# Kernel tuning notes

Measured on AMD Instinct MI355X. Metric: run time of the kernel, lower is better.

Reference implementation:

```python
import jax, jax.numpy as jnp
import numpy as np

B, N, FIN, D, L, DF = 16, 768, 56, 140, 4, 128


def setup_inputs() -> dict:
    key = jax.random.key(0)
    ks = jax.random.split(key, 24)
    c_hs = jax.random.normal(ks[0], (B, N, FIN), jnp.float32)
    # receptor prefix length r, total atoms n (r < n <= N)
    r = jax.random.randint(ks[1], (B,), N // 4, N // 2)
    num_atoms = jax.random.randint(ks[2], (B,), (3 * N) // 4, N + 1).astype(jnp.int32)
    idx = jnp.arange(N)
    c_valid = (idx[None, :] < r[:, None]).astype(jnp.int32)
    # intra-molecule adjacency: sparse symmetric 0/1 with self loops
    a1 = (jax.random.uniform(ks[3], (B, N, N)) < 0.05).astype(jnp.float32)
    c_adjs1 = jnp.clip(jnp.maximum(a1, a1.transpose(0, 2, 1)) + jnp.eye(N, dtype=jnp.float32)[None], 0.0, 1.0)
    # cross distances in Angstroms
    d2 = jax.random.uniform(ks[4], (B, N, N), jnp.float32, 0.0, 20.0)
    c_adjs2 = 0.5 * (d2 + d2.transpose(0, 2, 1))
    s = 0.1
    params = dict(
        W_emb=s * jax.random.normal(ks[5], (FIN, D), jnp.float32),
        gat_W=s * jax.random.normal(ks[6], (L, D, D), jnp.float32),
        gat_Wb=jnp.zeros((L, D), jnp.float32),
        gat_A=s * jax.random.normal(ks[7], (L, D, D), jnp.float32),
        gat_gw=s * jax.random.normal(ks[8], (L, 2 * D, 1), jnp.float32),
        gat_gb=jnp.zeros((L, 1), jnp.float32),
        fc_w0=s * jax.random.normal(ks[9], (D, DF), jnp.float32),
        fc_b0=jnp.zeros((DF,), jnp.float32),
        fc_w1=s * jax.random.normal(ks[10], (DF, DF), jnp.float32),
        fc_b1=jnp.zeros((DF,), jnp.float32),
        fc_w2=s * jax.random.normal(ks[11], (DF, DF), jnp.float32),
        fc_b2=jnp.zeros((DF,), jnp.float32),
        fc_w3=s * jax.random.normal(ks[12], (DF, 1), jnp.float32),
        fc_b3=jnp.zeros((1,), jnp.float32),
        mu=jnp.array([4.0], jnp.float32),
        dev=jnp.array([1.0], jnp.float32),
    )
    return dict(c_hs=c_hs, c_adjs1=c_adjs1, c_adjs2=c_adjs2, c_valid=c_valid, num_atoms=num_atoms, **params)


def _formulate_adj2(adj2, c_valid, num_atoms, mu, dev):
    # vectorized version of the per-batch Python loop in Formulate_Adj2
    r = jnp.sum(c_valid > 0, axis=1)          # [B] receptor prefix length
    n = num_atoms                              # [B] total atoms
    i = jnp.arange(N)
    row_rec = i[None, :, None] < r[:, None, None]              # row < r
    col_lig = (i[None, None, :] >= r[:, None, None]) & (i[None, None, :] < n[:, None, None])
    maskA = row_rec & col_lig                  # [B,N,N] receptor-row x ligand-col block
    gauss = jnp.exp(-jnp.square(adj2 - mu) / dev)
    upd = jnp.where(adj2 <= 10.0, gauss, jnp.zeros_like(adj2))
    out = jnp.where(maskA, upd, adj2)
    out = jnp.where(maskA.transpose(0, 2, 1), out.transpose(0, 2, 1), out)  # symmetrize block
    return out


def _gat_gate(x, adj, W, Wb, A, gw, gb):
    h = x @ W + Wb                                             # [B,N,D]
    e = jnp.einsum('bjl,bkl->bjk', h @ A, h)                   # [B,N,N]
    e = e + e.transpose(0, 2, 1)
    att = jnp.where(adj > 0, e, jnp.float32(-9e15))
    att = jax.nn.softmax(att, axis=1)                          # NOTE: dim=1, as in torch code
    att = att * adj
    h_prime = jax.nn.relu(jnp.einsum('bij,bjk->bik', att, h))  # [B,N,D]
    coeff = jax.nn.sigmoid(jnp.concatenate([x, h_prime], -1) @ gw + gb)  # [B,N,1]
    return coeff * x + (1.0 - coeff) * h_prime


def reference(c_hs, c_adjs1, c_adjs2, c_valid, num_atoms, W_emb, gat_W, gat_Wb, gat_A, gat_gw, gat_gb,
              fc_w0, fc_b0, fc_w1, fc_b1, fc_w2, fc_b2, fc_w3, fc_b3, mu, dev):
    x = c_hs @ W_emb                                           # embede (no bias)
    adj2 = _formulate_adj2(c_adjs2, c_valid, num_atoms, mu, dev)
    for k in range(gat_W.shape[0]):                            # embede_graph (eval: dropout is identity)
        h1 = _gat_gate(x, c_adjs1, gat_W[k], gat_Wb[k], gat_A[k], gat_gw[k], gat_gb[k])
        h2 = _gat_gate(x, adj2, gat_W[k], gat_Wb[k], gat_A[k], gat_gw[k], gat_gb[k])
        x = h2 - h1
    # Get_Prediction: ragged sum pool over first num_atoms rows
    mask = (jnp.arange(N)[None, :] < num_atoms[:, None]).astype(x.dtype)
    pred = jnp.sum(x * mask[:, :, None], axis=1)               # [B,D]
    h = jax.nn.relu(pred @ fc_w0 + fc_b0)
    h = jax.nn.relu(h @ fc_w1 + fc_b1)
    h = jax.nn.relu(h @ fc_w2 + fc_b2)
    out = jax.nn.sigmoid(h @ fc_w3 + fc_b3)
    return out.reshape(-1)                                     # [B]
```

## Files before the change

kernel.cpp:

```cpp
#include <hip/hip_runtime.h>

constexpr int B   = 16;
constexpr int N   = 768;
constexpr int FIN = 56;
constexpr int D   = 140;
constexpr int L   = 4;
constexpr int DF  = 128;
constexpr int NN  = N * N;
constexpr int BND = B * N * D;
constexpr int BNN = B * NN;

constexpr int PROWS  = 16;
constexpr int NCHUNK = N / PROWS;

constexpr int NTILE = N / 64;
constexpr int NTRI  = NTILE * (NTILE + 1) / 2;

constexpr int JSPLIT = 8;

struct PartPtrs { float* p[JSPLIT]; };

template<int K>
__global__ __launch_bounds__(256) void k_linrb(const float* __restrict__ in,
                                               const float* __restrict__ W,
                                               const float* __restrict__ bias,
                                               float* __restrict__ out) {
    constexpr int NDG = D / 4;
    int idx = blockIdx.x * 256 + threadIdx.x;
    if (idx >= (B * N / 4) * NDG) return;
    int dt = idx % NDG;
    int rt = idx / NDG;
    int r0 = rt * 4, d = dt * 4;

    float acc[4][4];
    float b0 = 0.f, b1 = 0.f, b2 = 0.f, b3 = 0.f;
    if (bias) { b0 = bias[d]; b1 = bias[d + 1]; b2 = bias[d + 2]; b3 = bias[d + 3]; }
#pragma unroll
    for (int s = 0; s < 4; ++s) {
        acc[s][0] = b0; acc[s][1] = b1; acc[s][2] = b2; acc[s][3] = b3;
    }

#pragma unroll 2
    for (int k = 0; k < K; k += 4) {
        float4 wv[4];
#pragma unroll
        for (int kk = 0; kk < 4; ++kk)
            wv[kk] = *reinterpret_cast<const float4*>(&W[(size_t)(k + kk) * D + d]);
#pragma unroll
        for (int s = 0; s < 4; ++s) {
            float4 xv = *reinterpret_cast<const float4*>(&in[(size_t)(r0 + s) * K + k]);
            float xa[4] = {xv.x, xv.y, xv.z, xv.w};
#pragma unroll
            for (int kk = 0; kk < 4; ++kk) {
                acc[s][0] += xa[kk] * wv[kk].x;
                acc[s][1] += xa[kk] * wv[kk].y;
                acc[s][2] += xa[kk] * wv[kk].z;
                acc[s][3] += xa[kk] * wv[kk].w;
            }
        }
    }

#pragma unroll
    for (int s = 0; s < 4; ++s) {
        float4 v = {acc[s][0], acc[s][1], acc[s][2], acc[s][3]};
        *reinterpret_cast<float4*>(&out[(size_t)(r0 + s) * D + d]) = v;
    }
}

__global__ __launch_bounds__(256) void k_adj2(const float* __restrict__ a2,
                                              const int* __restrict__ valid,
                                              const int* __restrict__ natoms,
                                              const float* __restrict__ mu,
                                              const float* __restrict__ dev,
                                              float* __restrict__ out) {
    int idx = blockIdx.x * 256 + threadIdx.x;
    if (idx >= BNN) return;
    int b   = idx / NN;
    int rem = idx - b * NN;
    int i   = rem / N;
    int j   = rem - i * N;
    float a = a2[idx];
    int vi = valid[b * N + i];
    int vj = valid[b * N + j];
    int n  = natoms[b];
    bool mask = (vi && !vj && (j < n)) || (vj && !vi && (i < n));
    float dmu = a - mu[0];
    float g = (a <= 10.f) ? expf(-dmu * dmu / dev[0]) : 0.f;
    out[idx] = mask ? g : a;
}

__global__ __launch_bounds__(256) void k_e(const float* __restrict__ h,
                                           const float* __restrict__ hA,
                                           float* __restrict__ E) {
    int t = blockIdx.x;
    int b = blockIdx.y;
    int tj = 0, rem = t, rowlen = NTILE;
    while (rem >= rowlen) { rem -= rowlen; ++tj; --rowlen; }
    int tk = tj + rem;

    __shared__ float sJ[72][68];
    __shared__ float sK[72][68];
    int tid = threadIdx.x;
    int jg  = tid & 15;
    int kg  = tid >> 4;
    int j0 = tj * 64, k0 = tk * 64;
    const float* hb = h  + (size_t)b * N * D;
    const float* ab = hA + (size_t)b * N * D;

    float acc[4][4] = {};

    for (int r = 0; r < 4; ++r) {
        int ph = r >> 1;
        int c0 = (r & 1) ? 72 : 0;
        int kc = (r & 1) ? 68 : 72;
        int ncb = kc >> 2;
        const float* uS = ph ? hb : ab;
        const float* vS = ph ? ab : hb;
        if (r) __syncthreads();
        for (int idx = tid; idx < ncb * 16; idx += 256) {
            int cb = idx % ncb;
            int jb = (idx / ncb) * 4;
            int gc = c0 + cb * 4;
            float4 ru[4], rv[4];
#pragma unroll
            for (int s = 0; s < 4; ++s) {
                ru[s] = *reinterpret_cast<const float4*>(&uS[(size_t)(j0 + jb + s) * D + gc]);
                rv[s] = *reinterpret_cast<const float4*>(&vS[(size_t)(k0 + jb + s) * D + gc]);
            }
            float tu[4][4], tv[4][4];
#pragma unroll
            for (int s = 0; s < 4; ++s) {
                tu[s][0] = ru[s].x; tu[s][1] = ru[s].y; tu[s][2] = ru[s].z; tu[s][3] = ru[s].w;
                tv[s][0] = rv[s].x; tv[s][1] = rv[s].y; tv[s][2] = rv[s].z; tv[s][3] = rv[s].w;
            }
#pragma unroll
            for (int s = 0; s < 4; ++s) {
                float4 wu = {tu[0][s], tu[1][s], tu[2][s], tu[3][s]};
                float4 wv = {tv[0][s], tv[1][s], tv[2][s], tv[3][s]};
                *reinterpret_cast<float4*>(&sJ[cb * 4 + s][jb]) = wu;
                *reinterpret_cast<float4*>(&sK[cb * 4 + s][jb]) = wv;
            }
        }
        __syncthreads();
#pragma unroll 4
        for (int kk = 0; kk < kc; ++kk) {
            float4 ajv = *reinterpret_cast<const float4*>(&sJ[kk][jg * 4]);
            float4 akv = *reinterpret_cast<const float4*>(&sK[kk][kg * 4]);
            float aj[4] = {ajv.x, ajv.y, ajv.z, ajv.w};
            float ak[4] = {akv.x, akv.y, akv.z, akv.w};
#pragma unroll
            for (int i = 0; i < 4; ++i)
#pragma unroll
                for (int q = 0; q < 4; ++q) acc[i][q] += aj[i] * ak[q];
        }
    }

    float* Eb = E + (size_t)b * NN;
    int jb = j0 + jg * 4, kb = k0 + kg * 4;
#pragma unroll
    for (int i = 0; i < 4; ++i) {
        float4 v = {acc[i][0], acc[i][1], acc[i][2], acc[i][3]};
        *reinterpret_cast<float4*>(&Eb[(size_t)(jb + i) * N + kb]) = v;
    }
#pragma unroll
    for (int q = 0; q < 4; ++q) {
        float4 v = {acc[0][q], acc[1][q], acc[2][q], acc[3][q]};
        *reinterpret_cast<float4*>(&Eb[(size_t)(kb + q) * N + jb]) = v;
    }
}

__global__ __launch_bounds__(1024) void k_stats(const float* __restrict__ E,
                                                const float* __restrict__ a1,
                                                const float* __restrict__ a2,
                                                float* __restrict__ M1g, float* __restrict__ IS1g,
                                                float* __restrict__ M2g, float* __restrict__ IS2g) {
    int b    = blockIdx.y;
    int lane = threadIdx.x & 63;
    int js   = threadIdx.x >> 6;
    int k    = blockIdx.x * 64 + lane;
    const float* Eb = E  + (size_t)b * NN;
    const float* A1 = a1 + (size_t)b * NN;
    const float* A2 = a2 + (size_t)b * NN;

    float m1 = -3.0e38f, s1 = 0.f, m2 = -3.0e38f, s2 = 0.f;
    for (int j = js; j < N; j += 16) {
        float ev = Eb[(size_t)j * N + k];
        float v1 = A1[(size_t)j * N + k];
        float v2 = A2[(size_t)j * N + k];
        float x1 = (v1 > 0.f) ? ev : -9e15f;
        float x2 = (v2 > 0.f) ? ev : -9e15f;
        float n1 = fmaxf(m1, x1);
        s1 = s1 * __expf(m1 - n1) + __expf(x1 - n1);
        m1 = n1;
        float n2 = fmaxf(m2, x2);
        s2 = s2 * __expf(m2 - n2) + __expf(x2 - n2);
        m2 = n2;
    }
    __shared__ float sm1[16][64], ss1[16][64], sm2[16][64], ss2[16][64];
    sm1[js][lane] = m1; ss1[js][lane] = s1;
    sm2[js][lane] = m2; ss2[js][lane] = s2;
    __syncthreads();
    if (js == 0) {
        float M = sm1[0][lane], S = ss1[0][lane];
#pragma unroll
        for (int q = 1; q < 16; ++q) {
            float mq = sm1[q][lane], sq = ss1[q][lane];
            float nm = fmaxf(M, mq);
            S = S * __expf(M - nm) + sq * __expf(mq - nm);
            M = nm;
        }
        M1g[(size_t)b * N + k] = M;
        IS1g[(size_t)b * N + k] = 1.f / S;
        M = sm2[0][lane]; S = ss2[0][lane];
#pragma unroll
        for (int q = 1; q < 16; ++q) {
            float mq = sm2[q][lane], sq = ss2[q][lane];
            float nm = fmaxf(M, mq);
            S = S * __expf(M - nm) + sq * __expf(mq - nm);
            M = nm;
        }
        M2g[(size_t)b * N + k] = M;
        IS2g[(size_t)b * N + k] = 1.f / S;
    }
}

__global__ __launch_bounds__(192) void k_athf(const float* __restrict__ E,
                                              const float* __restrict__ adj,
                                              const float* __restrict__ Mg,
                                              const float* __restrict__ ISg,
                                              const float* __restrict__ h,
                                              PartPtrs P) {
    int ti = blockIdx.x;
    int bz = blockIdx.y;
    int b  = bz >> 3;
    int js = bz & 7;
    __shared__ float sA[48][68];
    __shared__ float sM[96], sIS[96];
    int tid = threadIdx.x;
    int ig  = tid & 15;
    int dg  = tid >> 4;
    int i0  = ti * 64;
    const float* Eb = E   + (size_t)b * NN;
    const float* Ab = adj + (size_t)b * NN;
    const float* hb = h   + (size_t)b * N * D;
    int jbase = js * (N / JSPLIT);

    if (tid < 96) {
        sM[tid]  = Mg[(size_t)b * N + jbase + tid];
        sIS[tid] = ISg[(size_t)b * N + jbase + tid];
    }
    __syncthreads();

    float acc[4][12] = {};

    for (int jt = 0; jt < 2; ++jt) {
        int j0 = jbase + jt * 48;
        int jl = jt * 48;
        if (jt) __syncthreads();
        {
            int jb4 = tid % 12, ib4 = tid / 12;
            float4 ev[4], av[4];
#pragma unroll
            for (int s = 0; s < 4; ++s) {
                size_t off = (size_t)(i0 + ib4 * 4 + s) * N + (j0 + jb4 * 4);
                ev[s] = *reinterpret_cast<const float4*>(&Eb[off]);
                av[s] = *reinterpret_cast<const float4*>(&Ab[off]);
            }
            float mj[4], isj[4];
#pragma unroll
            for (int c = 0; c < 4; ++c) {
                mj[c]  = sM[jl + jb4 * 4 + c];
                isj[c] = sIS[jl + jb4 * 4 + c];
            }
            float at[4][4];
#pragma unroll
            for (int s = 0; s < 4; ++s) {
                float ea[4] = {ev[s].x, ev[s].y, ev[s].z, ev[s].w};
                float aa[4] = {av[s].x, av[s].y, av[s].z, av[s].w};
#pragma unroll
                for (int c = 0; c < 4; ++c)
                    at[s][c] = (aa[c] > 0.f)
                             ? __expf(ea[c] - mj[c]) * isj[c] * aa[c] : 0.f;
            }
#pragma unroll
            for (int c = 0; c < 4; ++c) {
                int row = jb4 * 4 + c;
                int col = (ib4 * 4) ^ (((row >> 2) & 7) << 2);
                float4 w = {at[0][c], at[1][c], at[2][c], at[3][c]};
                *reinterpret_cast<float4*>(&sA[row][col]) = w;
            }
        }
        __syncthreads();
#pragma unroll 2
        for (int kk = 0; kk < 48; ++kk) {
            int col = (ig * 4) ^ (((kk >> 2) & 7) << 2);
            float4 a4 = *reinterpret_cast<const float4*>(&sA[kk][col]);
            const float* hrow = hb + (size_t)(j0 + kk) * D + dg * 12;
            float4 h0 = *reinterpret_cast<const float4*>(&hrow[0]);
            float4 h1 = *reinterpret_cast<const float4*>(&hrow[4]);
            float4 h2 = *reinterpret_cast<const float4*>(&hrow[8]);
            float ai[4]  = {a4.x, a4.y, a4.z, a4.w};
            float hd[12] = {h0.x, h0.y, h0.z, h0.w,
                            h1.x, h1.y, h1.z, h1.w,
                            h2.x, h2.y, h2.z, h2.w};
#pragma unroll
            for (int i = 0; i < 4; ++i)
#pragma unroll
                for (int q = 0; q < 12; ++q) acc[i][q] += ai[i] * hd[q];
        }
    }

    float* dst = P.p[js] + (size_t)b * N * D;
#pragma unroll
    for (int s = 0; s < 4; ++s) {
        int row = i0 + ig * 4 + s;
#pragma unroll
        for (int t = 0; t < 3; ++t) {
            int cc = dg * 12 + t * 4;
            if (cc < D) {
                float4 v = {acc[s][t * 4], acc[s][t * 4 + 1],
                            acc[s][t * 4 + 2], acc[s][t * 4 + 3]};
                *reinterpret_cast<float4*>(&dst[(size_t)row * D + cc]) = v;
            }
        }
    }
}

__global__ __launch_bounds__(64) void k_gate(const float* __restrict__ x,
                                             PartPtrs P,
                                             const float* __restrict__ gw,
                                             const float* __restrict__ gb,
                                             float* __restrict__ g1,
                                             float* __restrict__ xout,
                                             int mode) {
    int row  = blockIdx.x;
    int lane = threadIdx.x;
    const float* xr = x + (size_t)row * D;
    const float* pp[JSPLIT];
#pragma unroll
    for (int e = 0; e < JSPLIT; ++e) pp[e] = P.p[e] + (size_t)row * D;
    float xv[3], hv[3];
    float part = 0.f;
#pragma unroll
    for (int q = 0; q < 3; ++q) {
        int d = lane + q * 64;
        xv[q] = 0.f; hv[q] = 0.f;
        if (d < D) {
            xv[q] = xr[d];
            float s = pp[0][d];
#pragma unroll
            for (int e = 1; e < JSPLIT; ++e) s += pp[e][d];
            hv[q] = fmaxf(s, 0.f);
            part += xv[q] * gw[d] + hv[q] * gw[D + d];
        }
    }
#pragma unroll
    for (int off = 32; off; off >>= 1) part += __shfl_xor(part, off);
    float c = 1.f / (1.f + __expf(-(part + gb[0])));
#pragma unroll
    for (int q = 0; q < 3; ++q) {
        int d = lane + q * 64;
        if (d < D) {
            float v = c * xv[q] + (1.f - c) * hv[q];
            if (mode == 0) g1[(size_t)row * D + d] = v;
            else           xout[(size_t)row * D + d] = v - g1[(size_t)row * D + d];
        }
    }
}

__global__ __launch_bounds__(256) void k_pool(const float* __restrict__ x,
                                              const int* __restrict__ natoms,
                                              float* __restrict__ part) {
    int c = blockIdx.x;
    int b = blockIdx.y;
    int tid = threadIdx.x;
    if (tid >= D) return;
    int n  = natoms[b];
    int r0 = c * PROWS;
    int r1 = min(r0 + PROWS, n);
    const float* xb = x + (size_t)b * N * D;
    float acc = 0.f;
    for (int r = r0; r < r1; ++r) acc += xb[(size_t)r * D + tid];
    part[((size_t)b * NCHUNK + c) * D + tid] = acc;
}

__global__ __launch_bounds__(256) void k_final(const float* __restrict__ part,
                                               const float* __restrict__ w0, const float* __restrict__ b0,
                                               const float* __restrict__ w1, const float* __restrict__ b1,
                                               const float* __restrict__ w2, const float* __restrict__ b2,
                                               const float* __restrict__ w3, const float* __restrict__ b3,
                                               float* __restrict__ out) {
    int b   = blockIdx.x;
    int tid = threadIdx.x;
    __shared__ float pred[D];
    __shared__ float h0[DF], h1[DF], h2[DF];
    if (tid < D) {
        float acc = 0.f;
        const float* pb = part + (size_t)b * NCHUNK * D;
#pragma unroll 8
        for (int c = 0; c < NCHUNK; ++c) acc += pb[(size_t)c * D + tid];
        pred[tid] = acc;
    }
    __syncthreads();
    if (tid < DF) {
        float acc = b0[tid];
#pragma unroll 4
        for (int i = 0; i < D; ++i) acc += pred[i] * w0[i * DF + tid];
        h0[tid] = fmaxf(acc, 0.f);
    }
    __syncthreads();
    if (tid < DF) {
        float acc = b1[tid];
#pragma unroll 4
        for (int i = 0; i < DF; ++i) acc += h0[i] * w1[i * DF + tid];
        h1[tid] = fmaxf(acc, 0.f);
    }
    __syncthreads();
    if (tid < DF) {
        float acc = b2[tid];
#pragma unroll 4
        for (int i = 0; i < DF; ++i) acc += h1[i] * w2[i * DF + tid];
        h2[tid] = fmaxf(acc, 0.f);
    }
    __syncthreads();
    if (tid == 0) {
        float acc = b3[0];
        for (int i = 0; i < DF; ++i) acc += h2[i] * w3[i];
        out[b] = 1.f / (1.f + expf(-acc));
    }
}

extern "C" void kernel_launch(void* const* d_in, const int* in_sizes, int n_in,
                              void* d_out, int out_size, void* d_ws, size_t ws_size,
                              hipStream_t stream) {
    const float* c_hs  = (const float*)d_in[0];
    const float* adj1  = (const float*)d_in[1];
    const float* c_a2  = (const float*)d_in[2];
    const int*   valid = (const int*)d_in[3];
    const int*   nat   = (const int*)d_in[4];
    const float* Wemb  = (const float*)d_in[5];
    const float* gatW  = (const float*)d_in[6];
    const float* gatWb = (const float*)d_in[7];
    const float* gatA  = (const float*)d_in[8];
    const float* gatgw = (const float*)d_in[9];
    const float* gatgb = (const float*)d_in[10];
    const float* w0 = (const float*)d_in[11];
    const float* b0 = (const float*)d_in[12];
    const float* w1 = (const float*)d_in[13];
    const float* b1 = (const float*)d_in[14];
    const float* w2 = (const float*)d_in[15];
    const float* b2 = (const float*)d_in[16];
    const float* w3 = (const float*)d_in[17];
    const float* b3 = (const float*)d_in[18];
    const float* mu  = (const float*)d_in[19];
    const float* dev = (const float*)d_in[20];
    float* out = (float*)d_out;

    float* ws    = (float*)d_ws;
    float* adj2f = ws;
    float* Ebuf  = adj2f + BNN;
    float* ATTws = Ebuf + BNN;
    float* x     = ATTws + BNN;
    float* h     = x + BND;
    float* hA    = h + BND;
    float* hp    = hA + BND;
    float* g1    = hp + BND;
    float* pC    = g1 + BND;
    float* pD    = pC + BND;
    float* p4 = ATTws;
    float* p5 = ATTws + (size_t)1 * BND;
    float* p6 = ATTws + (size_t)2 * BND;
    float* p7 = ATTws + (size_t)3 * BND;
    float* M1  = ATTws + (size_t)4 * BND;
    float* IS1 = M1 + (size_t)B * N;
    float* M2  = IS1 + (size_t)B * N;
    float* IS2 = M2 + (size_t)B * N;
    PartPtrs P;
    P.p[0] = hp; P.p[1] = hA; P.p[2] = pC; P.p[3] = pD;
    P.p[4] = p4; P.p[5] = p5; P.p[6] = p6; P.p[7] = p7;
    float* part  = Ebuf;

    constexpr int LIN_GRID = (B * N / 4) * (D / 4) / 256;

    k_linrb<FIN><<<LIN_GRID, 256, 0, stream>>>(c_hs, Wemb, nullptr, x);
    k_adj2<<<(BNN + 255) / 256, 256, 0, stream>>>(c_a2, valid, nat, mu, dev, adj2f);

    for (int l = 0; l < L; ++l) {
        const float* Wl  = gatW + (size_t)l * D * D;
        const float* Wbl = gatWb + (size_t)l * D;
        const float* Al  = gatA + (size_t)l * D * D;
        const float* gwl = gatgw + (size_t)l * 2 * D;
        const float* gbl = gatgb + l;

        k_linrb<D><<<LIN_GRID, 256, 0, stream>>>(x, Wl, Wbl, h);
        k_linrb<D><<<LIN_GRID, 256, 0, stream>>>(h, Al, nullptr, hA);
        k_e<<<dim3(NTRI, B), 256, 0, stream>>>(h, hA, Ebuf);

        k_stats<<<dim3(N / 64, B), 1024, 0, stream>>>(Ebuf, adj1, adj2f,
                                                      M1, IS1, M2, IS2);

        k_athf<<<dim3(NTILE, B * JSPLIT), 192, 0, stream>>>(Ebuf, adj1, M1, IS1,
                                                            h, P);
        k_gate<<<B * N, 64, 0, stream>>>(x, P, gwl, gbl, g1, nullptr, 0);

        k_athf<<<dim3(NTILE, B * JSPLIT), 192, 0, stream>>>(Ebuf, adj2f, M2, IS2,
                                                            h, P);
        k_gate<<<B * N, 64, 0, stream>>>(x, P, gwl, gbl, g1, x, 1);
    }

    k_pool<<<dim3(NCHUNK, B), 256, 0, stream>>>(x, nat, part);
    k_final<<<B, 256, 0, stream>>>(part, w0, b0, w1, b1, w2, b2, w3, b3, out);
}
```

Baseline: 1.488 ms.

## Halve attention j-split, enlarge j tiles, and prefetch h rows in k_athf

The attention-times-h kernel now splits the j dimension into 4 partitions instead of 8. Each block covers 192 j values in three 64-wide tiles, with the tile staging loop strided over 256 work items. The inner loop software-prefetches the next h row into registers while doing the FMAs on the current one. Fewer partial-sum buffers are written and reduced, but there are half as many blocks and more shared memory per block, which may reduce occupancy or parallelism.

```diff
diff --git a/kernel.cpp b/kernel.cpp
--- a/kernel.cpp
+++ b/kernel.cpp
@@ -16,7 +16,7 @@
 constexpr int NTILE = N / 64;
 constexpr int NTRI  = NTILE * (NTILE + 1) / 2;
 
-constexpr int JSPLIT = 8;
+constexpr int JSPLIT = 4;
 
 struct PartPtrs { float* p[JSPLIT]; };
 
@@ -232,10 +232,10 @@
                                               PartPtrs P) {
     int ti = blockIdx.x;
     int bz = blockIdx.y;
-    int b  = bz >> 3;
-    int js = bz & 7;
-    __shared__ float sA[48][68];
-    __shared__ float sM[96], sIS[96];
+    int b  = bz >> 2;
+    int js = bz & 3;
+    __shared__ float sA[64][68];
+    __shared__ float sM[192], sIS[192];
     int tid = threadIdx.x;
     int ig  = tid & 15;
     int dg  = tid >> 4;
@@ -245,20 +245,18 @@
     const float* hb = h   + (size_t)b * N * D;
     int jbase = js * (N / JSPLIT);
 
-    if (tid < 96) {
-        sM[tid]  = Mg[(size_t)b * N + jbase + tid];
-        sIS[tid] = ISg[(size_t)b * N + jbase + tid];
-    }
+    sM[tid]  = Mg[(size_t)b * N + jbase + tid];
+    sIS[tid] = ISg[(size_t)b * N + jbase + tid];
     __syncthreads();
 
     float acc[4][12] = {};
 
-    for (int jt = 0; jt < 2; ++jt) {
-        int j0 = jbase + jt * 48;
-        int jl = jt * 48;
+    for (int jt = 0; jt < 3; ++jt) {
+        int j0 = jbase + jt * 64;
+        int jl = jt * 64;
         if (jt) __syncthreads();
-        {
-            int jb4 = tid % 12, ib4 = tid / 12;
+        for (int idx = tid; idx < 256; idx += 192) {
+            int jb4 = idx & 15, ib4 = idx >> 4;
             float4 ev[4], av[4];
 #pragma unroll
             for (int s = 0; s < 4; ++s) {
@@ -291,14 +289,22 @@
             }
         }
         __syncthreads();
+
+        const float* hcol = hb + dg * 12;
+        const float* r0p = hcol + (size_t)j0 * D;
+        float4 nh0 = *reinterpret_cast<const float4*>(&r0p[0]);
+        float4 nh1 = *reinterpret_cast<const float4*>(&r0p[4]);
+        float4 nh2 = *reinterpret_cast<const float4*>(&r0p[8]);
 #pragma unroll 2
-        for (int kk = 0; kk < 48; ++kk) {
+        for (int kk = 0; kk < 64; ++kk) {
+            float4 h0 = nh0, h1 = nh1, h2 = nh2;
+            int nk = (kk < 63) ? kk + 1 : 63;
+            const float* nrp = hcol + (size_t)(j0 + nk) * D;
+            nh0 = *reinterpret_cast<const float4*>(&nrp[0]);
+            nh1 = *reinterpret_cast<const float4*>(&nrp[4]);
+            nh2 = *reinterpret_cast<const float4*>(&nrp[8]);
             int col = (ig * 4) ^ (((kk >> 2) & 7) << 2);
             float4 a4 = *reinterpret_cast<const float4*>(&sA[kk][col]);
-            const float* hrow = hb + (size_t)(j0 + kk) * D + dg * 12;
-            float4 h0 = *reinterpret_cast<const float4*>(&hrow[0]);
-            float4 h1 = *reinterpret_cast<const float4*>(&hrow[4]);
-            float4 h2 = *reinterpret_cast<const float4*>(&hrow[8]);
             float ai[4]  = {a4.x, a4.y, a4.z, a4.w};
             float hd[12] = {h0.x, h0.y, h0.z, h0.w,
                             h1.x, h1.y, h1.z, h1.w,
@@ -467,17 +473,12 @@
     float* g1    = hp + BND;
     float* pC    = g1 + BND;
     float* pD    = pC + BND;
-    float* p4 = ATTws;
-    float* p5 = ATTws + (size_t)1 * BND;
-    float* p6 = ATTws + (size_t)2 * BND;
-    float* p7 = ATTws + (size_t)3 * BND;
-    float* M1  = ATTws + (size_t)4 * BND;
-    float* IS1 = M1 + (size_t)B * N;
-    float* M2  = IS1 + (size_t)B * N;
-    float* IS2 = M2 + (size_t)B * N;
+    float* M1  = ATTws;
+    float* IS1 = ATTws + (size_t)B * N;
+    float* M2  = ATTws + (size_t)2 * B * N;
+    float* IS2 = ATTws + (size_t)3 * B * N;
     PartPtrs P;
     P.p[0] = hp; P.p[1] = hA; P.p[2] = pC; P.p[3] = pD;
-    P.p[4] = p4; P.p[5] = p5; P.p[6] = p6; P.p[7] = p7;
     float* part  = Ebuf;
 
     constexpr int LIN_GRID = (B * N / 4) * (D / 4) / 256;
```

Result: faster. 1.403 ms (-5.7%).

## Fuse both adjacency attention passes into one kernel sharing E and h loads

Applied to the files above, without the earlier changes.

The two attention-times-h kernels (for adj1 and adj2) are merged into one kernel that reads the energy matrix and h once and accumulates both products. The two gate kernels merge into one that computes both gates and writes x directly. JSPLIT drops from 8 to 4 with 64-wide j tiles, which halves the partial buffers read by the gate. The cost is double the accumulator registers and shared memory per block, plus fewer blocks in the grid, which can lower occupancy and parallelism.

```diff
diff --git a/kernel.cpp b/kernel.cpp
--- a/kernel.cpp
+++ b/kernel.cpp
@@ -16,9 +16,9 @@
 constexpr int NTILE = N / 64;
 constexpr int NTRI  = NTILE * (NTILE + 1) / 2;
 
-constexpr int JSPLIT = 8;
-
-struct PartPtrs { float* p[JSPLIT]; };
+constexpr int JSPLIT = 4;
+
+struct GatePtrs { float* g1[JSPLIT]; float* g2[JSPLIT]; };
 
 template<int K>
 __global__ __launch_bounds__(256) void k_linrb(const float* __restrict__ in,
@@ -224,93 +224,114 @@
     }
 }
 
-__global__ __launch_bounds__(192) void k_athf(const float* __restrict__ E,
-                                              const float* __restrict__ adj,
-                                              const float* __restrict__ Mg,
-                                              const float* __restrict__ ISg,
-                                              const float* __restrict__ h,
-                                              PartPtrs P) {
+__global__ __launch_bounds__(192) void k_athf2(const float* __restrict__ E,
+                                               const float* __restrict__ adj1,
+                                               const float* __restrict__ adj2,
+                                               const float* __restrict__ M1g,
+                                               const float* __restrict__ IS1g,
+                                               const float* __restrict__ M2g,
+                                               const float* __restrict__ IS2g,
+                                               const float* __restrict__ h,
+                                               GatePtrs P) {
     int ti = blockIdx.x;
     int bz = blockIdx.y;
-    int b  = bz >> 3;
-    int js = bz & 7;
-    __shared__ float sA[48][68];
-    __shared__ float sM[96], sIS[96];
+    int b  = bz >> 2;
+    int js = bz & 3;
+    __shared__ float sA1[64][68];
+    __shared__ float sA2[64][68];
+    __shared__ float sM1[192], sIS1[192], sM2[192], sIS2[192];
     int tid = threadIdx.x;
     int ig  = tid & 15;
     int dg  = tid >> 4;
     int i0  = ti * 64;
-    const float* Eb = E   + (size_t)b * NN;
-    const float* Ab = adj + (size_t)b * NN;
-    const float* hb = h   + (size_t)b * N * D;
+    const float* Eb = E    + (size_t)b * NN;
+    const float* A1 = adj1 + (size_t)b * NN;
+    const float* A2 = adj2 + (size_t)b * NN;
+    const float* hb = h    + (size_t)b * N * D;
     int jbase = js * (N / JSPLIT);
 
-    if (tid < 96) {
-        sM[tid]  = Mg[(size_t)b * N + jbase + tid];
-        sIS[tid] = ISg[(size_t)b * N + jbase + tid];
-    }
+    sM1[tid]  = M1g[(size_t)b * N + jbase + tid];
+    sIS1[tid] = IS1g[(size_t)b * N + jbase + tid];
+    sM2[tid]  = M2g[(size_t)b * N + jbase + tid];
+    sIS2[tid] = IS2g[(size_t)b * N + jbase + tid];
     __syncthreads();
 
-    float acc[4][12] = {};
-
-    for (int jt = 0; jt < 2; ++jt) {
-        int j0 = jbase + jt * 48;
-        int jl = jt * 48;
+    float ac1[4][12] = {};
+    float ac2[4][12] = {};
+
+    for (int jt = 0; jt < 3; ++jt) {
+        int j0 = jbase + jt * 64;
+        int jl = jt * 64;
         if (jt) __syncthreads();
-        {
-            int jb4 = tid % 12, ib4 = tid / 12;
-            float4 ev[4], av[4];
+        for (int idx = tid; idx < 256; idx += 192) {
+            int jb4 = idx & 15, ib4 = idx >> 4;
+            float4 ev[4], a1v[4], a2v[4];
 #pragma unroll
             for (int s = 0; s < 4; ++s) {
                 size_t off = (size_t)(i0 + ib4 * 4 + s) * N + (j0 + jb4 * 4);
-                ev[s] = *reinterpret_cast<const float4*>(&Eb[off]);
-                av[s] = *reinterpret_cast<const float4*>(&Ab[off]);
-            }
-            float mj[4], isj[4];
+                ev[s]  = *reinterpret_cast<const float4*>(&Eb[off]);
+                a1v[s] = *reinterpret_cast<const float4*>(&A1[off]);
+                a2v[s] = *reinterpret_cast<const float4*>(&A2[off]);
+            }
+            float mj1[4], is1[4], mj2[4], is2[4];
 #pragma unroll
             for (int c = 0; c < 4; ++c) {
-                mj[c]  = sM[jl + jb4 * 4 + c];
-                isj[c] = sIS[jl + jb4 * 4 + c];
-            }
-            float at[4][4];
+                mj1[c] = sM1[jl + jb4 * 4 + c];
+                is1[c] = sIS1[jl + jb4 * 4 + c];
+                mj2[c] = sM2[jl + jb4 * 4 + c];
+                is2[c] = sIS2[jl + jb4 * 4 + c];
+            }
+            float t1[4][4], t2[4][4];
 #pragma unroll
             for (int s = 0; s < 4; ++s) {
                 float ea[4] = {ev[s].x, ev[s].y, ev[s].z, ev[s].w};
-                float aa[4] = {av[s].x, av[s].y, av[s].z, av[s].w};
-#pragma unroll
-                for (int c = 0; c < 4; ++c)
-                    at[s][c] = (aa[c] > 0.f)
-                             ? __expf(ea[c] - mj[c]) * isj[c] * aa[c] : 0.f;
+                float b1[4] = {a1v[s].x, a1v[s].y, a1v[s].z, a1v[s].w};
+                float b2[4] = {a2v[s].x, a2v[s].y, a2v[s].z, a2v[s].w};
+#pragma unroll
+                for (int c = 0; c < 4; ++c) {
+                    t1[s][c] = (b1[c] > 0.f)
+                             ? __expf(ea[c] - mj1[c]) * is1[c] * b1[c] : 0.f;
+                    t2[s][c] = (b2[c] > 0.f)
+                             ? __expf(ea[c] - mj2[c]) * is2[c] * b2[c] : 0.f;
+                }
             }
 #pragma unroll
             for (int c = 0; c < 4; ++c) {
                 int row = jb4 * 4 + c;
                 int col = (ib4 * 4) ^ (((row >> 2) & 7) << 2);
-                float4 w = {at[0][c], at[1][c], at[2][c], at[3][c]};
-                *reinterpret_cast<float4*>(&sA[row][col]) = w;
+                float4 w1 = {t1[0][c], t1[1][c], t1[2][c], t1[3][c]};
+                float4 w2 = {t2[0][c], t2[1][c], t2[2][c], t2[3][c]};
+                *reinterpret_cast<float4*>(&sA1[row][col]) = w1;
+                *reinterpret_cast<float4*>(&sA2[row][col]) = w2;
             }
         }
         __syncthreads();
 #pragma unroll 2
-        for (int kk = 0; kk < 48; ++kk) {
+        for (int kk = 0; kk < 64; ++kk) {
             int col = (ig * 4) ^ (((kk >> 2) & 7) << 2);
-            float4 a4 = *reinterpret_cast<const float4*>(&sA[kk][col]);
+            float4 a4 = *reinterpret_cast<const float4*>(&sA1[kk][col]);
+            float4 b4 = *reinterpret_cast<const float4*>(&sA2[kk][col]);
             const float* hrow = hb + (size_t)(j0 + kk) * D + dg * 12;
             float4 h0 = *reinterpret_cast<const float4*>(&hrow[0]);
             float4 h1 = *reinterpret_cast<const float4*>(&hrow[4]);
             float4 h2 = *reinterpret_cast<const float4*>(&hrow[8]);
             float ai[4]  = {a4.x, a4.y, a4.z, a4.w};
+            float bi[4]  = {b4.x, b4.y, b4.z, b4.w};
             float hd[12] = {h0.x, h0.y, h0.z, h0.w,
                             h1.x, h1.y, h1.z, h1.w,
                             h2.x, h2.y, h2.z, h2.w};
 #pragma unroll
             for (int i = 0; i < 4; ++i)
 #pragma unroll
-                for (int q = 0; q < 12; ++q) acc[i][q] += ai[i] * hd[q];
-        }
-    }
-
-    float* dst = P.p[js] + (size_t)b * N * D;
+                for (int q = 0; q < 12; ++q) {
+                    ac1[i][q] += ai[i] * hd[q];
+                    ac2[i][q] += bi[i] * hd[q];
+                }
+        }
+    }
+
+    float* d1 = P.g1[js] + (size_t)b * N * D;
+    float* d2 = P.g2[js] + (size_t)b * N * D;
 #pragma unroll
     for (int s = 0; s < 4; ++s) {
         int row = i0 + ig * 4 + s;
@@ -318,52 +339,65 @@
         for (int t = 0; t < 3; ++t) {
             int cc = dg * 12 + t * 4;
             if (cc < D) {
-                float4 v = {acc[s][t * 4], acc[s][t * 4 + 1],
-                            acc[s][t * 4 + 2], acc[s][t * 4 + 3]};
-                *reinterpret_cast<float4*>(&dst[(size_t)row * D + cc]) = v;
-            }
-        }
-    }
-}
-
-__global__ __launch_bounds__(64) void k_gate(const float* __restrict__ x,
-                                             PartPtrs P,
-                                             const float* __restrict__ gw,
-                                             const float* __restrict__ gb,
-                                             float* __restrict__ g1,
-                                             float* __restrict__ xout,
-                                             int mode) {
+                float4 v1 = {ac1[s][t * 4], ac1[s][t * 4 + 1],
+                             ac1[s][t * 4 + 2], ac1[s][t * 4 + 3]};
+                float4 v2 = {ac2[s][t * 4], ac2[s][t * 4 + 1],
+                             ac2[s][t * 4 + 2], ac2[s][t * 4 + 3]};
+                *reinterpret_cast<float4*>(&d1[(size_t)row * D + cc]) = v1;
+                *reinterpret_cast<float4*>(&d2[(size_t)row * D + cc]) = v2;
+            }
+        }
+    }
+}
+
+__global__ __launch_bounds__(64) void k_gate2(float* __restrict__ x,
+                                              GatePtrs P,
+                                              const float* __restrict__ gw,
+                                              const float* __restrict__ gb) {
     int row  = blockIdx.x;
     int lane = threadIdx.x;
-    const float* xr = x + (size_t)row * D;
-    const float* pp[JSPLIT];
-#pragma unroll
-    for (int e = 0; e < JSPLIT; ++e) pp[e] = P.p[e] + (size_t)row * D;
-    float xv[3], hv[3];
-    float part = 0.f;
+    float* xr = x + (size_t)row * D;
+    const float* q1[JSPLIT];
+    const float* q2[JSPLIT];
+#pragma unroll
+    for (int e = 0; e < JSPLIT; ++e) {
+        q1[e] = P.g1[e] + (size_t)row * D;
+        q2[e] = P.g2[e] + (size_t)row * D;
+    }
+    float xv[3], h1v[3], h2v[3];
+    float p1 = 0.f, p2 = 0.f;
 #pragma unroll
     for (int q = 0; q < 3; ++q) {
         int d = lane + q * 64;
-        xv[q] = 0.f; hv[q] = 0.f;
+        xv[q] = 0.f; h1v[q] = 0.f; h2v[q] = 0.f;
         if (d < D) {
             xv[q] = xr[d];
-            float s = pp[0][d];
-#pragma unroll
-            for (int e = 1; e < JSPLIT; ++e) s += pp[e][d];
-            hv[q] = fmaxf(s, 0.f);
-            part += xv[q] * gw[d] + hv[q] * gw[D + d];
-        }
-    }
-#pragma unroll
-    for (int off = 32; off; off >>= 1) part += __shfl_xor(part, off);
-    float c = 1.f / (1.f + __expf(-(part + gb[0])));
+            float s1 = q1[0][d];
+#pragma unroll
+            for (int e = 1; e < JSPLIT; ++e) s1 += q1[e][d];
+            h1v[q] = fmaxf(s1, 0.f);
+            float s2 = q2[0][d];
+#pragma unroll
+            for (int e = 1; e < JSPLIT; ++e) s2 += q2[e][d];
+            h2v[q] = fmaxf(s2, 0.f);
+            p1 += xv[q] * gw[d] + h1v[q] * gw[D + d];
+            p2 += xv[q] * gw[d] + h2v[q] * gw[D + d];
+        }
+    }
+#pragma unroll
+    for (int off = 32; off; off >>= 1) {
+        p1 += __shfl_xor(p1, off);
+        p2 += __shfl_xor(p2, off);
+    }
+    float c1 = 1.f / (1.f + __expf(-(p1 + gb[0])));
+    float c2 = 1.f / (1.f + __expf(-(p2 + gb[0])));
 #pragma unroll
     for (int q = 0; q < 3; ++q) {
         int d = lane + q * 64;
         if (d < D) {
-            float v = c * xv[q] + (1.f - c) * hv[q];
-            if (mode == 0) g1[(size_t)row * D + d] = v;
-            else           xout[(size_t)row * D + d] = v - g1[(size_t)row * D + d];
+            float v1 = c1 * xv[q] + (1.f - c1) * h1v[q];
+            float v2 = c2 * xv[q] + (1.f - c2) * h2v[q];
+            xr[d] = v2 - v1;
         }
     }
 }
@@ -475,9 +509,9 @@
     float* IS1 = M1 + (size_t)B * N;
     float* M2  = IS1 + (size_t)B * N;
     float* IS2 = M2 + (size_t)B * N;
-    PartPtrs P;
-    P.p[0] = hp; P.p[1] = hA; P.p[2] = pC; P.p[3] = pD;
-    P.p[4] = p4; P.p[5] = p5; P.p[6] = p6; P.p[7] = p7;
+    GatePtrs P;
+    P.g1[0] = hp; P.g1[1] = hA; P.g1[2] = g1; P.g1[3] = pC;
+    P.g2[0] = p4; P.g2[1] = p5; P.g2[2] = p6; P.g2[3] = p7;
     float* part  = Ebuf;
 
     constexpr int LIN_GRID = (B * N / 4) * (D / 4) / 256;
@@ -499,13 +533,10 @@
         k_stats<<<dim3(N / 64, B), 1024, 0, stream>>>(Ebuf, adj1, adj2f,
                                                       M1, IS1, M2, IS2);
 
-        k_athf<<<dim3(NTILE, B * JSPLIT), 192, 0, stream>>>(Ebuf, adj1, M1, IS1,
-                                                            h, P);
-        k_gate<<<B * N, 64, 0, stream>>>(x, P, gwl, gbl, g1, nullptr, 0);
-
-        k_athf<<<dim3(NTILE, B * JSPLIT), 192, 0, stream>>>(Ebuf, adj2f, M2, IS2,
-                                                            h, P);
-        k_gate<<<B * N, 64, 0, stream>>>(x, P, gwl, gbl, g1, x, 1);
+        k_athf2<<<dim3(NTILE, B * JSPLIT), 192, 0, stream>>>(Ebuf, adj1, adj2f,
+                                                             M1, IS1, M2, IS2,
+                                                             h, P);
+        k_gate2<<<B * N, 64, 0, stream>>>(x, P, gwl, gbl);
     }
 
     k_pool<<<dim3(NCHUNK, B), 256, 0, stream>>>(x, nat, part);
```

After: 1.362 ms. 1.09x faster.
